# Kernel optimization log

Hardware: AMD Instinct MI355X
Metric: run time of the kernel (lower is better)

The kernel has to match this reference:

```python
import jax, jax.numpy as jnp
import numpy as np

WS = (2, 7, 7)      # window size
SS = (1, 3, 3)      # shift size
NH = 8              # num heads
DIM = 256
N = WS[0] * WS[1] * WS[2]   # 98 tokens per window
EPS = 1e-5


def _ln(x, w, b):
    m = jnp.mean(x, -1, keepdims=True)
    v = jnp.mean((x - m) ** 2, -1, keepdims=True)
    return (x - m) / jnp.sqrt(v + EPS) * w + b


def _rel_index():
    coords = np.stack(np.meshgrid(np.arange(WS[0]), np.arange(WS[1]), np.arange(WS[2]), indexing='ij'))
    cf = coords.reshape(3, -1)
    rc = (cf[:, :, None] - cf[:, None, :]).transpose(1, 2, 0).astype(np.int64)
    rc[..., 0] += WS[0] - 1
    rc[..., 1] += WS[1] - 1
    rc[..., 2] += WS[2] - 1
    rc[..., 0] *= (2 * WS[1] - 1) * (2 * WS[2] - 1)
    rc[..., 1] *= 2 * WS[2] - 1
    return rc.sum(-1).astype(np.int32)  # [N, N]


def _attn_mask(Dp, Hp, Wp):
    img = np.zeros((1, Dp, Hp, Wp, 1), np.float32)
    cnt = 0
    def sl(ws, ss):
        return (slice(0, -ws), slice(-ws, -ss), slice(-ss, None))
    for d in sl(WS[0], SS[0]):
        for h in sl(WS[1], SS[1]):
            for w in sl(WS[2], SS[2]):
                img[:, d, h, w, :] = cnt
                cnt += 1
    mw = img.reshape(1, Dp // WS[0], WS[0], Hp // WS[1], WS[1], Wp // WS[2], WS[2], 1)
    mw = mw.transpose(0, 1, 3, 5, 2, 4, 6, 7).reshape(-1, N)
    am = mw[:, None, :] - mw[:, :, None]
    return np.where(am != 0, np.float32(-100.0), np.float32(0.0)).astype(np.float32)  # [nW, N, N]


def setup_inputs() -> dict:
    key = jax.random.key(0)
    ks = jax.random.split(key, 6)
    B, D, H, W, C = 2, 16, 56, 56, DIM
    hid = 4 * C
    return {
        'x': jax.random.normal(ks[0], (B, D, H, W, C), jnp.float32),
        'mask_matrix': jnp.asarray(_attn_mask(D, H, W)),
        'rel_index': jnp.asarray(_rel_index()),
        'rel_bias_table': 0.02 * jax.random.normal(ks[1], ((2 * WS[0] - 1) * (2 * WS[1] - 1) * (2 * WS[2] - 1), NH), jnp.float32),
        'norm1_w': jnp.ones((C,), jnp.float32), 'norm1_b': jnp.zeros((C,), jnp.float32),
        'qkv_w': 0.02 * jax.random.normal(ks[2], (3 * C, C), jnp.float32), 'qkv_b': jnp.zeros((3 * C,), jnp.float32),
        'proj_w': 0.02 * jax.random.normal(ks[3], (C, C), jnp.float32), 'proj_b': jnp.zeros((C,), jnp.float32),
        'norm2_w': jnp.ones((C,), jnp.float32), 'norm2_b': jnp.zeros((C,), jnp.float32),
        'fc1_w': 0.02 * jax.random.normal(ks[4], (hid, C), jnp.float32), 'fc1_b': jnp.zeros((hid,), jnp.float32),
        'fc2_w': 0.02 * jax.random.normal(ks[5], (C, hid), jnp.float32), 'fc2_b': jnp.zeros((C,), jnp.float32),
    }


def _forward(x, mask_matrix, rel_index, rel_bias_table, norm1_w, norm1_b, qkv_w, qkv_b,
             proj_w, proj_b, norm2_w, norm2_b, fc1_w, fc1_b, fc2_w, fc2_b):
    B, D, H, W, C = x.shape
    nh, hd = NH, C // NH
    scale = hd ** -0.5
    nd, nhw, nww = D // WS[0], H // WS[1], W // WS[2]

    # --- part 1: norm -> shift -> window attention -> unshift ---
    h = _ln(x, norm1_w, norm1_b)
    h = jnp.roll(h, (-SS[0], -SS[1], -SS[2]), axis=(1, 2, 3))
    # window partition -> [B_, N, C]
    h = h.reshape(B, nd, WS[0], nhw, WS[1], nww, WS[2], C)
    h = h.transpose(0, 1, 3, 5, 2, 4, 6, 7).reshape(-1, N, C)
    B_ = h.shape[0]

    qkv = (h @ qkv_w.T + qkv_b).reshape(B_, N, 3, nh, hd).transpose(2, 0, 3, 1, 4)
    q, k, v = qkv[0], qkv[1], qkv[2]   # [B_, nh, N, hd]
    attn = jnp.einsum('bhnd,bhmd->bhnm', q * scale, k)
    bias = rel_bias_table[rel_index.reshape(-1)].reshape(N, N, nh).transpose(2, 0, 1)
    attn = attn + bias[None]
    nW = mask_matrix.shape[0]
    attn = attn.reshape(B_ // nW, nW, nh, N, N) + mask_matrix[None, :, None]
    attn = jax.nn.softmax(attn.reshape(B_, nh, N, N), axis=-1)
    o = jnp.einsum('bhnm,bhmd->bhnd', attn, v).transpose(0, 2, 1, 3).reshape(B_, N, C)
    o = o @ proj_w.T + proj_b
    # window reverse -> [B, D, H, W, C]
    o = o.reshape(B, nd, nhw, nww, WS[0], WS[1], WS[2], C)
    o = o.transpose(0, 1, 4, 2, 5, 3, 6, 7).reshape(B, D, H, W, C)
    o = jnp.roll(o, SS, axis=(1, 2, 3))

    x = x + o
    # --- part 2: MLP ---
    h2 = _ln(x, norm2_w, norm2_b)
    h2 = jax.nn.gelu(h2 @ fc1_w.T + fc1_b, approximate=False)
    return x + (h2 @ fc2_w.T + fc2_b)


def reference(x, mask_matrix, rel_index, rel_bias_table, norm1_w, norm1_b, qkv_w, qkv_b,
              proj_w, proj_b, norm2_w, norm2_b, fc1_w, fc1_b, fc2_w, fc2_b):
    return _forward(x, mask_matrix, rel_index, rel_bias_table, norm1_w, norm1_b, qkv_w, qkv_b,
                    proj_w, proj_b, norm2_w, norm2_b, fc1_w, fc1_b, fc2_w, fc2_b)
```

## Files before the change

### kernel.cpp

```cpp
#include <hip/hip_runtime.h>
#include <hip/hip_bf16.h>

typedef __attribute__((ext_vector_type(8))) short bf16x8;
typedef __attribute__((ext_vector_type(4))) float f32x4;

__device__ __forceinline__ unsigned short f2bf(float f){
  __hip_bfloat16 h = __float2bfloat16(f);
  return *reinterpret_cast<unsigned short*>(&h);
}
__device__ __forceinline__ float bf2f(unsigned short u){
  unsigned int v = ((unsigned int)u) << 16;
  return __uint_as_float(v);
}

#define GLDS16(gptr, lptr) \
  __builtin_amdgcn_global_load_lds((const __attribute__((address_space(1))) unsigned int*)(gptr), \
                                   (__attribute__((address_space(3))) unsigned int*)(lptr), 16, 0, 0)

__global__ void cvtk(const float* __restrict__ s, unsigned short* __restrict__ d, int n){
  int i = blockIdx.x*256 + threadIdx.x;
  if (i < n) d[i] = f2bf(s[i]);
}

__global__ void combok(const int* __restrict__ ri, const float* __restrict__ tbl,
                       const float* __restrict__ mask, unsigned short* __restrict__ out){
  int g = blockIdx.x*256 + threadIdx.x;
  if (g >= 802816) return;
  int r = g & 3;
  int t = g >> 2;
  int lane = t & 63; t >>= 6;
  int nt = t % 7; t /= 7;
  int mt = t % 7; t /= 7;
  int p = t >> 3, h = t & 7;
  int gi = mt*16 + (lane >> 4)*4 + r; if (gi > 97) gi = 97;
  int j  = nt*16 + (lane & 15);
  float v;
  if (j < 98){
    int wrep = ((p&4)?448:0) + ((p&2)?56:0) + ((p&1)?7:0);
    v = tbl[ri[gi*98 + j]*8 + h] + mask[(size_t)wrep*9604 + gi*98 + j];
  } else {
    v = -30000.f;
  }
  out[g] = f2bf(v);
}

__launch_bounds__(256)
__global__ void lnk(const float* __restrict__ xin, const float* __restrict__ gw, const float* __restrict__ gb,
                    unsigned short* __restrict__ hout, int mode)
{
  int wid = threadIdx.x >> 6, lane = threadIdx.x & 63;
  int tok = blockIdx.x*4 + wid;
  int src;
  if (mode == 0){
    int w = tok / 98, n = tok % 98;
    int b = w >> 9, rr = w & 511;
    int di = rr >> 6, hi = (rr >> 3) & 7, wi = rr & 7;
    int d2 = n / 49, n2 = n % 49, h2 = n2 / 7, w2 = n2 % 7;
    int sd = (di*2 + d2 + 1) & 15;
    int sh = hi*7 + h2 + 3; if (sh >= 56) sh -= 56;
    int sw = wi*7 + w2 + 3; if (sw >= 56) sw -= 56;
    src = ((b*16 + sd)*56 + sh)*56 + sw;
  } else {
    src = tok;
  }
  float4 v = *(const float4*)(xin + (size_t)src*256 + lane*4);
  float s  = v.x + v.y + v.z + v.w;
  float s2 = v.x*v.x + v.y*v.y + v.z*v.z + v.w*v.w;
  #pragma unroll
  for (int off = 1; off < 64; off <<= 1){
    s  += __shfl_xor(s, off);
    s2 += __shfl_xor(s2, off);
  }
  float mean = s * (1.f/256.f);
  float var  = s2 * (1.f/256.f) - mean*mean;
  float rstd = rsqrtf(var + 1e-5f);
  int c = lane*4;
  float4 wv = *(const float4*)(gw + c);
  float4 bv = *(const float4*)(gb + c);
  unsigned int p0 = (unsigned int)f2bf((v.x-mean)*rstd*wv.x + bv.x)
                  | ((unsigned int)f2bf((v.y-mean)*rstd*wv.y + bv.y) << 16);
  unsigned int p1 = (unsigned int)f2bf((v.z-mean)*rstd*wv.z + bv.z)
                  | ((unsigned int)f2bf((v.w-mean)*rstd*wv.w + bv.w) << 16);
  uint2 pk; pk.x = p0; pk.y = p1;
  *(uint2*)(hout + (size_t)tok*256 + c) = pk;
}

template<int EPI>
__launch_bounds__(256, 2)
__global__ void gemmk(const unsigned short* __restrict__ A, const unsigned short* __restrict__ Bw,
                      const float* __restrict__ bias, int K, int nbx,
                      unsigned short* __restrict__ outb, const float* __restrict__ xres,
                      float* __restrict__ outf, int moff)
{
  __shared__ unsigned short As[128*32];
  __shared__ unsigned short Bs[128*32];
  int tid = threadIdx.x;
  int wid = tid >> 6, lane = tid & 63, l16 = lane & 15, lk = lane >> 4;
  int wm = wid >> 1, wn = wid & 1;
  int cpx = gridDim.x >> 3;
  int swb = (blockIdx.x & 7)*cpx + (blockIdx.x >> 3);
  int mblk = swb / nbx, nblk = swb % nbx;
  const unsigned short* Ab = A  + (size_t)mblk*128*K;
  const unsigned short* Bb = Bw + (size_t)nblk*128*K;
  int rA = tid >> 2, kcA = (tid & 3)*8;

  f32x4 acc[4][4];
  #pragma unroll
  for (int i = 0; i < 4; i++)
    #pragma unroll
    for (int j = 0; j < 4; j++)
      acc[i][j] = (f32x4){0.f,0.f,0.f,0.f};

  for (int ks = 0; ks < K; ks += 32){
    __syncthreads();
    GLDS16(Ab + (size_t)rA*K      + ks + kcA, &As[wid*512]);
    GLDS16(Ab + (size_t)(rA+64)*K + ks + kcA, &As[2048 + wid*512]);
    GLDS16(Bb + (size_t)rA*K      + ks + kcA, &Bs[wid*512]);
    GLDS16(Bb + (size_t)(rA+64)*K + ks + kcA, &Bs[2048 + wid*512]);
    __syncthreads();
    bf16x8 af[4], bfr[4];
    #pragma unroll
    for (int mi = 0; mi < 4; mi++) af[mi]  = *(const bf16x8*)&As[(wm*64 + mi*16 + l16)*32 + lk*8];
    #pragma unroll
    for (int ni = 0; ni < 4; ni++) bfr[ni] = *(const bf16x8*)&Bs[(wn*64 + ni*16 + l16)*32 + lk*8];
    #pragma unroll
    for (int mi = 0; mi < 4; mi++)
      #pragma unroll
      for (int ni = 0; ni < 4; ni++)
        acc[mi][ni] = __builtin_amdgcn_mfma_f32_16x16x32_bf16(af[mi], bfr[ni], acc[mi][ni], 0, 0, 0);
  }

  int rowb = mblk*128 + wm*64;
  int colb = nblk*128 + wn*64;
  #pragma unroll
  for (int mi = 0; mi < 4; mi++){
    #pragma unroll
    for (int r = 0; r < 4; r++){
      int row = rowb + mi*16 + lk*4 + r;
      if constexpr (EPI == 0){
        int w = row / 98, n = row % 98;
        size_t obase = ((size_t)w*8)*3136 + (size_t)n*32;
        #pragma unroll
        for (int ni = 0; ni < 4; ni++){
          int col = colb + ni*16 + l16;
          float v = acc[mi][ni][r] + bias[col];
          int which = col >> 8, head = (col >> 5) & 7, e = col & 31;
          if (which == 0) v *= 0.17677669529663687f;
          outb[(size_t)which*25690112 + obase + (size_t)head*3136 + e] = f2bf(v);
        }
      } else if constexpr (EPI == 1){
        int w = row / 98, n = row % 98;
        int b = w >> 9, rr = w & 511;
        int di = rr >> 6, hi = (rr >> 3) & 7, wi = rr & 7;
        int d2 = n / 49, n2 = n % 49, h2 = n2 / 7, w2 = n2 % 7;
        int sd = (di*2 + d2 + 1) & 15;
        int sh = hi*7 + h2 + 3; if (sh >= 56) sh -= 56;
        int sw = wi*7 + w2 + 3; if (sw >= 56) sw -= 56;
        size_t tnat = (((size_t)b*16 + sd)*56 + sh)*56 + sw;
        #pragma unroll
        for (int ni = 0; ni < 4; ni++){
          int col = colb + ni*16 + l16;
          float v = acc[mi][ni][r] + bias[col];
          outf[tnat*256 + col] = xres[tnat*256 + col] + v;
        }
      } else if constexpr (EPI == 2){
        #pragma unroll
        for (int ni = 0; ni < 4; ni++){
          int col = colb + ni*16 + l16;
          float v = acc[mi][ni][r] + bias[col];
          float gl = v * 0.5f * (1.f + erff(v * 0.70710678118654752f));
          outb[(size_t)row*1024 + col] = f2bf(gl);
        }
      } else {
        #pragma unroll
        for (int ni = 0; ni < 4; ni++){
          int col = colb + ni*16 + l16;
          float v = acc[mi][ni][r] + bias[col];
          outf[((size_t)(moff + row))*256 + col] += v;
        }
      }
    }
  }
}

__launch_bounds__(256)
__global__ void attnk(const unsigned short* __restrict__ qkv, const unsigned short* __restrict__ comboX,
                      unsigned short* __restrict__ obuf)
{
  __shared__ unsigned short P[4][16*136];
  int tid = threadIdx.x, wid = tid >> 6, lane = tid & 63, l16 = lane & 15, lk = lane >> 4;
  int cpx = gridDim.x >> 3;
  int swb = (blockIdx.x & 7)*cpx + (blockIdx.x >> 3);
  int task = swb*4 + wid;
  int w = task >> 3, h = task & 7;
  int rr = w & 511;
  int pat = (((rr>>6)==7)?4:0) | ((((rr>>3)&7)==7)?2:0) | (((rr&7)==7)?1:0);
  const unsigned short* cb = comboX + (size_t)(pat*8 + h)*12544;
  const unsigned short* qb = qkv + ((size_t)w*8 + h)*3136;
  const unsigned short* kb = qb + 25690112;
  const unsigned short* vb = kb + 25690112;

  bf16x8 v0[4], v1[4];
  #pragma unroll
  for (int kcc = 0; kcc < 4; kcc++){
    #pragma unroll
    for (int j = 0; j < 8; j++){
      int k = kcc*32 + lk*8 + j; if (k > 97) k = 97;
      v0[kcc][j] = (short)vb[k*32 + l16];
      v1[kcc][j] = (short)vb[k*32 + 16 + l16];
    }
  }

  unsigned short* Pw = &P[wid][0];
  { int rp = lane >> 2, cc = 112 + (lane & 3)*4;
    *(uint2*)&Pw[rp*136 + cc] = make_uint2(0u, 0u); }

  for (int mt = 0; mt < 7; mt++){
    int qrow = mt*16 + l16; if (qrow > 97) qrow = 97;
    bf16x8 qa = *(const bf16x8*)(qb + qrow*32 + lk*8);

    f32x4 s[7];
    #pragma unroll
    for (int nt = 0; nt < 7; nt++){
      int kc = nt*16 + l16; if (kc > 97) kc = 97;
      bf16x8 kf = *(const bf16x8*)(kb + kc*32 + lk*8);
      f32x4 z = (f32x4){0.f,0.f,0.f,0.f};
      s[nt] = __builtin_amdgcn_mfma_f32_16x16x32_bf16(qa, kf, z, 0, 0, 0);
    }

    const unsigned short* cm = cb + mt*1792;
    float mx[4] = {-3e38f,-3e38f,-3e38f,-3e38f};
    #pragma unroll
    for (int nt = 0; nt < 7; nt++){
      uint2 c2 = *(const uint2*)(cm + (nt*64 + lane)*4);
      s[nt][0] += bf2f((unsigned short)(c2.x & 0xffff));
      s[nt][1] += bf2f((unsigned short)(c2.x >> 16));
      s[nt][2] += bf2f((unsigned short)(c2.y & 0xffff));
      s[nt][3] += bf2f((unsigned short)(c2.y >> 16));
      mx[0] = fmaxf(mx[0], s[nt][0]); mx[1] = fmaxf(mx[1], s[nt][1]);
      mx[2] = fmaxf(mx[2], s[nt][2]); mx[3] = fmaxf(mx[3], s[nt][3]);
    }
    #pragma unroll
    for (int r = 0; r < 4; r++){
      #pragma unroll
      for (int off = 1; off < 16; off <<= 1) mx[r] = fmaxf(mx[r], __shfl_xor(mx[r], off));
    }
    float sm[4] = {0.f,0.f,0.f,0.f};
    #pragma unroll
    for (int r = 0; r < 4; r++){
      #pragma unroll
      for (int nt = 0; nt < 7; nt++){
        float e = __expf(s[nt][r] - mx[r]);
        s[nt][r] = e; sm[r] += e;
      }
    }
    #pragma unroll
    for (int r = 0; r < 4; r++){
      #pragma unroll
      for (int off = 1; off < 16; off <<= 1) sm[r] += __shfl_xor(sm[r], off);
      sm[r] = 1.f / sm[r];
    }

    #pragma unroll
    for (int r = 0; r < 4; r++)
      #pragma unroll
      for (int nt = 0; nt < 7; nt++)
        Pw[(lk*4 + r)*136 + nt*16 + l16] = f2bf(s[nt][r]*sm[r]);

    f32x4 o0 = (f32x4){0.f,0.f,0.f,0.f}, o1 = (f32x4){0.f,0.f,0.f,0.f};
    #pragma unroll
    for (int kcc = 0; kcc < 4; kcc++){
      bf16x8 pa = *(const bf16x8*)&Pw[l16*136 + kcc*32 + lk*8];
      o0 = __builtin_amdgcn_mfma_f32_16x16x32_bf16(pa, v0[kcc], o0, 0, 0, 0);
      o1 = __builtin_amdgcn_mfma_f32_16x16x32_bf16(pa, v1[kcc], o1, 0, 0, 0);
    }
    #pragma unroll
    for (int r = 0; r < 4; r++){
      int n = mt*16 + lk*4 + r;
      if (n < 98){
        size_t ob = ((size_t)w*98 + n)*256 + h*32;
        obuf[ob + l16]      = f2bf(o0[r]);
        obuf[ob + 16 + l16] = f2bf(o1[r]);
      }
    }
  }
}

extern "C" void kernel_launch(void* const* d_in, const int* in_sizes, int n_in,
                              void* d_out, int out_size, void* d_ws, size_t ws_size,
                              hipStream_t stream)
{
  const float* x     = (const float*)d_in[0];
  const float* maskm = (const float*)d_in[1];
  const int*   ri    = (const int*)d_in[2];
  const float* tbl   = (const float*)d_in[3];
  const float* n1w   = (const float*)d_in[4];
  const float* n1b   = (const float*)d_in[5];
  const float* qkvw  = (const float*)d_in[6];
  const float* qkvbv = (const float*)d_in[7];
  const float* projw = (const float*)d_in[8];
  const float* projb = (const float*)d_in[9];
  const float* n2w   = (const float*)d_in[10];
  const float* n2b   = (const float*)d_in[11];
  const float* fc1w  = (const float*)d_in[12];
  const float* fc1b  = (const float*)d_in[13];
  const float* fc2w  = (const float*)d_in[14];
  const float* fc2b  = (const float*)d_in[15];
  float* dout = (float*)d_out;
  char* ws = (char*)d_ws;

  unsigned short* qkvB  = (unsigned short*)(ws + 0);
  unsigned short* hb    = (unsigned short*)(ws + 154140672);
  unsigned short* wq    = (unsigned short*)(ws + 205520896);
  unsigned short* comboX= (unsigned short*)(ws + 205914112);
  unsigned short* wp    = (unsigned short*)(ws + 0);
  unsigned short* h2 = (unsigned short*)(ws + 0);
  unsigned short* g  = (unsigned short*)(ws + 51380224);
  unsigned short* w1 = (unsigned short*)(ws + 102760448);
  unsigned short* w2 = (unsigned short*)(ws + 103284736);

  cvtk<<<768, 256, 0, stream>>>(qkvw, wq, 196608);
  combok<<<3136, 256, 0, stream>>>(ri, tbl, maskm, comboX);

  lnk<<<25088, 256, 0, stream>>>(x, n1w, n1b, hb, 0);
  gemmk<0><<<784*6, 256, 0, stream>>>(hb, wq, qkvbv, 256, 6, qkvB, nullptr, nullptr, 0);
  attnk<<<2048, 256, 0, stream>>>(qkvB, comboX, hb);
  cvtk<<<256, 256, 0, stream>>>(projw, wp, 65536);
  gemmk<1><<<784*2, 256, 0, stream>>>(hb, wp, projb, 256, 2, nullptr, x, dout, 0);

  cvtk<<<1024, 256, 0, stream>>>(fc1w, w1, 262144);
  cvtk<<<1024, 256, 0, stream>>>(fc2w, w2, 262144);
  lnk<<<25088, 256, 0, stream>>>(dout, n2w, n2b, h2, 1);
  for (int c = 0; c < 4; c++){
    gemmk<2><<<196*8, 256, 0, stream>>>(h2 + (size_t)c*25088*256, w1, fc1b, 256, 8, g, nullptr, nullptr, 0);
    gemmk<3><<<196*2, 256, 0, stream>>>(g, w2, fc2b, 1024, 2, nullptr, nullptr, dout, c*25088);
  }
}
```

Before: 528.7 us.

## Store QKV token-major and fold bias-mask into attention MFMA accumulator

The QKV GEMM epilogue now writes a plain row-major [token, 768] bf16 buffer instead of scattering into head-major q/k/v planes. The attention kernel reads q, k and v with a 768-element row stride. V columns are loaded as interleaved pairs, so each output store becomes one packed 32-bit write. The relative-bias-plus-mask term now seeds the QK MFMA accumulator instead of being added afterwards, and s_setprio raises wave priority around the PV MFMAs. The aim is cheaper epilogue address math and fewer ALU ops in attention, at the cost of more strided, less contiguous attention loads.

```diff
diff --git a/kernel.cpp b/kernel.cpp
--- a/kernel.cpp
+++ b/kernel.cpp
@@ -7,10 +7,6 @@
 __device__ __forceinline__ unsigned short f2bf(float f){
   __hip_bfloat16 h = __float2bfloat16(f);
   return *reinterpret_cast<unsigned short*>(&h);
-}
-__device__ __forceinline__ float bf2f(unsigned short u){
-  unsigned int v = ((unsigned int)u) << 16;
-  return __uint_as_float(v);
 }
 
 #define GLDS16(gptr, lptr) \
@@ -138,15 +134,12 @@
     for (int r = 0; r < 4; r++){
       int row = rowb + mi*16 + lk*4 + r;
       if constexpr (EPI == 0){
-        int w = row / 98, n = row % 98;
-        size_t obase = ((size_t)w*8)*3136 + (size_t)n*32;
         #pragma unroll
         for (int ni = 0; ni < 4; ni++){
           int col = colb + ni*16 + l16;
           float v = acc[mi][ni][r] + bias[col];
-          int which = col >> 8, head = (col >> 5) & 7, e = col & 31;
-          if (which == 0) v *= 0.17677669529663687f;
-          outb[(size_t)which*25690112 + obase + (size_t)head*3136 + e] = f2bf(v);
+          if (col < 256) v *= 0.17677669529663687f;
+          outb[(size_t)row*768 + col] = f2bf(v);
         }
       } else if constexpr (EPI == 1){
         int w = row / 98, n = row % 98;
@@ -196,9 +189,7 @@
   int rr = w & 511;
   int pat = (((rr>>6)==7)?4:0) | ((((rr>>3)&7)==7)?2:0) | (((rr&7)==7)?1:0);
   const unsigned short* cb = comboX + (size_t)(pat*8 + h)*12544;
-  const unsigned short* qb = qkv + ((size_t)w*8 + h)*3136;
-  const unsigned short* kb = qb + 25690112;
-  const unsigned short* vb = kb + 25690112;
+  const unsigned short* base = qkv + (size_t)w*98*768 + h*32;
 
   bf16x8 v0[4], v1[4];
   #pragma unroll
@@ -206,8 +197,9 @@
     #pragma unroll
     for (int j = 0; j < 8; j++){
       int k = kcc*32 + lk*8 + j; if (k > 97) k = 97;
-      v0[kcc][j] = (short)vb[k*32 + l16];
-      v1[kcc][j] = (short)vb[k*32 + 16 + l16];
+      unsigned int u = *(const unsigned int*)(base + (size_t)k*768 + 512 + 2*l16);
+      v0[kcc][j] = (short)(u & 0xffff);
+      v1[kcc][j] = (short)(u >> 16);
     }
   }
 
@@ -217,26 +209,26 @@
 
   for (int mt = 0; mt < 7; mt++){
     int qrow = mt*16 + l16; if (qrow > 97) qrow = 97;
-    bf16x8 qa = *(const bf16x8*)(qb + qrow*32 + lk*8);
-
+    bf16x8 qa = *(const bf16x8*)(base + (size_t)qrow*768 + lk*8);
+
+    const unsigned short* cm = cb + mt*1792;
     f32x4 s[7];
     #pragma unroll
     for (int nt = 0; nt < 7; nt++){
       int kc = nt*16 + l16; if (kc > 97) kc = 97;
-      bf16x8 kf = *(const bf16x8*)(kb + kc*32 + lk*8);
-      f32x4 z = (f32x4){0.f,0.f,0.f,0.f};
-      s[nt] = __builtin_amdgcn_mfma_f32_16x16x32_bf16(qa, kf, z, 0, 0, 0);
-    }
-
-    const unsigned short* cm = cb + mt*1792;
+      bf16x8 kf = *(const bf16x8*)(base + (size_t)kc*768 + 256 + lk*8);
+      uint2 c2 = *(const uint2*)(cm + (nt*64 + lane)*4);
+      f32x4 ci;
+      ci[0] = __uint_as_float(c2.x << 16);
+      ci[1] = __uint_as_float(c2.x & 0xffff0000u);
+      ci[2] = __uint_as_float(c2.y << 16);
+      ci[3] = __uint_as_float(c2.y & 0xffff0000u);
+      s[nt] = __builtin_amdgcn_mfma_f32_16x16x32_bf16(qa, kf, ci, 0, 0, 0);
+    }
+
     float mx[4] = {-3e38f,-3e38f,-3e38f,-3e38f};
     #pragma unroll
     for (int nt = 0; nt < 7; nt++){
-      uint2 c2 = *(const uint2*)(cm + (nt*64 + lane)*4);
-      s[nt][0] += bf2f((unsigned short)(c2.x & 0xffff));
-      s[nt][1] += bf2f((unsigned short)(c2.x >> 16));
-      s[nt][2] += bf2f((unsigned short)(c2.y & 0xffff));
-      s[nt][3] += bf2f((unsigned short)(c2.y >> 16));
       mx[0] = fmaxf(mx[0], s[nt][0]); mx[1] = fmaxf(mx[1], s[nt][1]);
       mx[2] = fmaxf(mx[2], s[nt][2]); mx[3] = fmaxf(mx[3], s[nt][3]);
     }
@@ -271,16 +263,17 @@
     #pragma unroll
     for (int kcc = 0; kcc < 4; kcc++){
       bf16x8 pa = *(const bf16x8*)&Pw[l16*136 + kcc*32 + lk*8];
+      __builtin_amdgcn_s_setprio(1);
       o0 = __builtin_amdgcn_mfma_f32_16x16x32_bf16(pa, v0[kcc], o0, 0, 0, 0);
       o1 = __builtin_amdgcn_mfma_f32_16x16x32_bf16(pa, v1[kcc], o1, 0, 0, 0);
+      __builtin_amdgcn_s_setprio(0);
     }
     #pragma unroll
     for (int r = 0; r < 4; r++){
       int n = mt*16 + lk*4 + r;
       if (n < 98){
-        size_t ob = ((size_t)w*98 + n)*256 + h*32;
-        obuf[ob + l16]      = f2bf(o0[r]);
-        obuf[ob + 16 + l16] = f2bf(o1[r]);
+        unsigned int pk = (unsigned int)f2bf(o0[r]) | ((unsigned int)f2bf(o1[r]) << 16);
+        *(unsigned int*)(obuf + ((size_t)w*98 + n)*256 + h*32 + 2*l16) = pk;
       }
     }
   }
```

Result: faster. 513.3 us (-2.9%).
